# Optimization experiments

Measured on AMD Instinct MI355X. Metric: run time of the kernel, lower is better.

## Reference

```python
import jax, jax.numpy as jnp
import numpy as np

N, E, H, D_IN, D_OUT, DEPTH, G = 100000, 1600000, 128, 128, 10, 3, 256


def setup_inputs() -> dict:
    key = jax.random.key(0)
    ks = jax.random.split(key, 16)
    s = lambda k, shape: jax.random.normal(k, shape, dtype=jnp.float32) * 0.05
    inp = {
        "x": jax.random.normal(ks[0], (N, D_IN), dtype=jnp.float32),
        "edge_index": jax.random.randint(ks[1], (2, E), 0, N, dtype=jnp.int32),
        "control_edge_index": jax.random.randint(ks[2], (2, 1024), 0, N, dtype=jnp.int32),
        "batch": jnp.sort(jax.random.randint(ks[3], (N,), 0, G, dtype=jnp.int32)),
        # encoder MLP: input_dim -> hidden -> hidden
        "enc_w1": s(ks[4], (D_IN, H)), "enc_b1": jnp.zeros((H,), jnp.float32),
        "enc_w2": s(ks[5], (H, H)),    "enc_b2": jnp.zeros((H,), jnp.float32),
        # conv_depth GCN layers, hidden -> hidden
        "conv_w": s(ks[6], (DEPTH, H, H)), "conv_b": jnp.zeros((DEPTH, H), jnp.float32),
        # decoder MLP: hidden -> hidden -> output_dim
        "dec_w1": s(ks[7], (H, H)),     "dec_b1": jnp.zeros((H,), jnp.float32),
        "dec_w2": s(ks[8], (H, D_OUT)), "dec_b2": jnp.zeros((D_OUT,), jnp.float32),
    }
    return inp


def _gcn_forward(x, enc_w1, enc_b1, enc_w2, enc_b2, conv_w, conv_b,
                 dec_w1, dec_b1, dec_w2, dec_b2, edge_index, batch):
    # encoder MLP (Linear-ReLU-Dropout(eval)-Linear)
    h = jax.nn.relu(x @ enc_w1 + enc_b1) @ enc_w2 + enc_b2

    # GCN normalization with self-loops: D^{-1/2} (A + I) D^{-1/2}
    loops = jnp.arange(N, dtype=edge_index.dtype)
    src = jnp.concatenate([edge_index[0], loops])  # [E + N]
    dst = jnp.concatenate([edge_index[1], loops])
    deg = jax.ops.segment_sum(jnp.ones_like(src, dtype=h.dtype), dst, num_segments=N)
    inv_sqrt = jax.lax.rsqrt(deg)  # deg >= 1 thanks to self-loops
    coef = (inv_sqrt[src] * inv_sqrt[dst])[:, None]  # [E+N, 1]

    for l in range(DEPTH):
        hw = h @ conv_w[l] + conv_b[l]                      # [N, H]
        h = jax.ops.segment_sum(hw[src] * coef, dst, num_segments=N)
        if l < DEPTH - 1:  # linear=False -> nonlinearity between convs
            h = jax.nn.relu(h)

    # global_add_pool over graph ids
    pooled = jax.ops.segment_sum(h, batch, num_segments=G)   # [G, H]

    # decoder MLP
    return jax.nn.relu(pooled @ dec_w1 + dec_b1) @ dec_w2 + dec_b2  # [G, D_OUT]


def reference(x, edge_index, control_edge_index, batch, enc_w1, enc_b1, enc_w2,
              enc_b2, conv_w, conv_b, dec_w1, dec_b1, dec_w2, dec_b2):
    # control_edge_index corresponds to the (disabled) control mechanism; unused
    return _gcn_forward(x, enc_w1, enc_b1, enc_w2, enc_b2, conv_w, conv_b,
                        dec_w1, dec_b1, dec_w2, dec_b2, edge_index, batch)
```

## Files before the change

### kernel.cpp

```cpp
#include <hip/hip_runtime.h>
#include <hip/hip_bf16.h>
#include <cstdint>
#include <cstddef>

#define NN 100000
#define NE 1600000
#define HH 128
#define NG 256

#define NB 196
#define BSH 9
#define BMSK 511
#define CHUNK 16384
#define NBLK 98

typedef __bf16 bf16x8 __attribute__((ext_vector_type(8)));
typedef float floatx4 __attribute__((ext_vector_type(4)));

__device__ __forceinline__ uint32_t f2b(float f) {
  union { float f; uint32_t u; } v; v.f = f;
  uint32_t u = v.u;
  return (u + 0x7FFFu + ((u >> 16) & 1u)) >> 16;
}
__device__ __forceinline__ float b2f(uint32_t h) {
  union { uint32_t u; float f; } v; v.u = h << 16;
  return v.f;
}
__device__ __forceinline__ void addrow(float* a, uint4 v) {
  a[0] += b2f(v.x & 0xFFFFu); a[1] += b2f(v.x >> 16);
  a[2] += b2f(v.y & 0xFFFFu); a[3] += b2f(v.y >> 16);
  a[4] += b2f(v.z & 0xFFFFu); a[5] += b2f(v.z >> 16);
  a[6] += b2f(v.w & 0xFFFFu); a[7] += b2f(v.w >> 16);
}

__device__ __forceinline__ void stage_w(uint16_t (*Wt)[136], const float* __restrict__ W,
                                        int tid) {
  for (int it = 0; it < 16; ++it) {
    int idx = tid + it * 256;
    int n = idx & 127;
    int k0 = (idx >> 7) * 4;
    uint2 wv;
    wv.x = f2b(W[(k0 + 0) * 128 + n]) | (f2b(W[(k0 + 1) * 128 + n]) << 16);
    wv.y = f2b(W[(k0 + 2) * 128 + n]) | (f2b(W[(k0 + 3) * 128 + n]) << 16);
    *(uint2*)&Wt[n][k0] = wv;
  }
}


__global__ __launch_bounds__(256) void k_cntA(const int* __restrict__ src,
                                              int* __restrict__ blkcnt) {
  __shared__ int h[NB];
  int t = threadIdx.x;
  if (t < NB) h[t] = 0;
  __syncthreads();
  int base = blockIdx.x * CHUNK, end = min(base + CHUNK, NE);
  for (int i = base + t; i < end; i += 256) atomicAdd(&h[src[i] >> BSH], 1);
  __syncthreads();
  if (t < NB) blkcnt[blockIdx.x * NB + t] = h[t];
}

__global__ __launch_bounds__(256) void k_cntB(const uint2* __restrict__ pairs,
                                              int* __restrict__ blkcnt) {
  __shared__ int h[NB];
  int t = threadIdx.x;
  if (t < NB) h[t] = 0;
  __syncthreads();
  int base = blockIdx.x * CHUNK, end = min(base + CHUNK, NE);
  for (int i = base + t; i < end; i += 256) atomicAdd(&h[pairs[i].y >> BSH], 1);
  __syncthreads();
  if (t < NB) blkcnt[blockIdx.x * NB + t] = h[t];
}

__global__ void k_scan(const int* __restrict__ blkcnt, int* __restrict__ poff,
                       int* __restrict__ gbase, int* __restrict__ off, int set_off) {
  __shared__ int s[256];
  int t = threadIdx.x;
  int tot = 0;
  if (t < NB) {
    for (int r = 0; r < NBLK; ++r) {
      poff[r * NB + t] = tot;
      tot += blkcnt[r * NB + t];
    }
  }
  s[t] = (t < NB) ? tot : 0;
  __syncthreads();
  for (int d = 1; d < 256; d <<= 1) {
    int v = (t >= d) ? s[t - d] : 0;
    __syncthreads();
    s[t] += v;
    __syncthreads();
  }
  if (t < NB) gbase[t] = s[t] - tot;
  if (t == 0) { gbase[NB] = NE; if (set_off) off[NN] = NE; }
}

__global__ __launch_bounds__(256) void k_placeA(const int* __restrict__ src,
                                                const int* __restrict__ dst,
                                                const int* __restrict__ poff,
                                                const int* __restrict__ gbase,
                                                uint2* __restrict__ pairs) {
  __shared__ int cur[NB];
  int t = threadIdx.x;
  if (t < NB) cur[t] = poff[blockIdx.x * NB + t] + gbase[t];
  __syncthreads();
  int base = blockIdx.x * CHUNK, end = min(base + CHUNK, NE);
  for (int i = base + t; i < end; i += 256) {
    int s = src[i], d = dst[i];
    int p = atomicAdd(&cur[s >> BSH], 1);
    pairs[p] = make_uint2((unsigned)s, (unsigned)d);
  }
}

__global__ __launch_bounds__(256) void k_placeB(const uint2* __restrict__ pairs,
                                                const int* __restrict__ poff,
                                                const int* __restrict__ gbase,
                                                uint32_t* __restrict__ outb) {
  __shared__ int cur[NB];
  int t = threadIdx.x;
  if (t < NB) cur[t] = poff[blockIdx.x * NB + t] + gbase[t];
  __syncthreads();
  int base = blockIdx.x * CHUNK, end = min(base + CHUNK, NE);
  for (int i = base + t; i < end; i += 256) {
    uint2 v = pairs[i];
    int p = atomicAdd(&cur[v.y >> BSH], 1);
    outb[p] = v.x | ((v.y & (unsigned)BMSK) << 17);
  }
}

__global__ __launch_bounds__(256) void k_bucket_sort(
    const uint32_t* __restrict__ pairbuf, const int* __restrict__ gbase,
    const int* __restrict__ batch,
    int* __restrict__ off, float* __restrict__ inv, int* __restrict__ csrs,
    int* __restrict__ dhist2, int* __restrict__ gstart)
{
  __shared__ int cnt[512];
  __shared__ int loff[512];
  __shared__ int psum[256];
  int b = blockIdx.x;
  int tid = threadIdx.x;
  cnt[tid] = 0; cnt[tid + 256] = 0;
  __syncthreads();
  int s0 = gbase[b], s1 = gbase[b + 1];
  for (int i = s0 + tid; i < s1; i += 256)
    atomicAdd(&cnt[pairbuf[i] >> 17], 1);
  __syncthreads();
  int a0 = cnt[2 * tid], a1 = cnt[2 * tid + 1];
  int s = a0 + a1;
  psum[tid] = s;
  __syncthreads();
  for (int d = 1; d < 256; d <<= 1) {
    int v = (tid >= d) ? psum[tid - d] : 0;
    __syncthreads();
    psum[tid] += v;
    __syncthreads();
  }
  int excl = psum[tid] - s;
  loff[2 * tid] = excl;
  loff[2 * tid + 1] = excl + a0;
  __syncthreads();
  int* h64 = psum;
  if (tid < 64) h64[tid] = 0;
  __syncthreads();
#pragma unroll
  for (int k = 0; k < 2; ++k) {
    int i = tid + k * 256;
    int node = b * 512 + i;
    if (node < NN) {
      off[node] = s0 + loff[i];
      inv[node] = rsqrtf((float)cnt[i] + 1.0f);
      int d = cnt[i]; if (d > 63) d = 63;
      atomicAdd(&h64[d], 1);
    }
  }
  {
    int n0 = b * 512, n1 = min(n0 + 512, NN);
    for (int i = n0 + tid; i < n1; i += 256) {
      int bb = batch[i];
      if (i == 0) { for (int g = 0; g <= bb; ++g) gstart[g] = 0; }
      else { int aa = batch[i - 1]; for (int g = aa + 1; g <= bb; ++g) gstart[g] = i; }
      if (i == NN - 1) { for (int g = bb + 1; g <= NG; ++g) gstart[g] = NN; }
    }
  }
  __syncthreads();
  if (tid < 64) dhist2[b * 64 + tid] = h64[tid];
  cnt[tid] = loff[tid]; cnt[tid + 256] = loff[tid + 256];
  __syncthreads();
  for (int i = s0 + tid; i < s1; i += 256) {
    uint32_t v = pairbuf[i];
    int p = atomicAdd(&cnt[v >> 17], 1);
    csrs[s0 + p] = (int)(v & 0x1FFFFu);
  }
}

__global__ void k_dscan(const int* __restrict__ dhist2, int* __restrict__ dcur) {
  int t = threadIdx.x;
  int sum = 0;
  for (int r = 0; r < NB; ++r) sum += dhist2[r * 64 + (63 - t)];
  int v = sum;
  for (int d = 1; d < 64; d <<= 1) { int u = __shfl_up(v, d); if (t >= d) v += u; }
  dcur[63 - t] = v - sum;
}

__global__ __launch_bounds__(256) void k_dplace(const int* __restrict__ off,
                                                int* __restrict__ dcur,
                                                int* __restrict__ order) {
  __shared__ int h[64], base[64];
  int t = threadIdx.x;
  if (t < 64) h[t] = 0;
  __syncthreads();
  int i = blockIdx.x * 256 + t;
  int d = 0, ld = 0;
  if (i < NN) { d = off[i + 1] - off[i]; if (d > 63) d = 63; ld = atomicAdd(&h[d], 1); }
  __syncthreads();
  if (t < 64) base[t] = h[t] ? atomicAdd(&dcur[t], h[t]) : 0;
  __syncthreads();
  if (i < NN) order[base[d] + ld] = i;
}

__global__ __launch_bounds__(256) void k_gemm(
    const uint16_t* __restrict__ A16, const float* __restrict__ A32,
    const float* __restrict__ W, const float* __restrict__ bias,
    const float* __restrict__ scale,
    uint16_t* __restrict__ Out, int M, int do_relu)
{
  __shared__ uint16_t Wt[128][136];
  const int tid = threadIdx.x;
  stage_w(Wt, W, tid);
  __syncthreads();

  const int lane = tid & 63;
  const int wave = tid >> 6;
  const int lrow = lane & 15;
  const int quad = lane >> 4;
  const int lk = quad * 8;
  const int row0 = blockIdx.x * 128 + wave * 32;

  floatx4 acc[2][8];
#pragma unroll
  for (int t = 0; t < 2; ++t)
#pragma unroll
    for (int n = 0; n < 8; ++n)
      acc[t][n] = (floatx4){0.f, 0.f, 0.f, 0.f};

#pragma unroll
  for (int ks = 0; ks < 4; ++ks) {
    bf16x8 a[2];
#pragma unroll
    for (int t = 0; t < 2; ++t) {
      int r = row0 + t * 16 + lrow;
      uint4 tmp = {0u, 0u, 0u, 0u};
      if (r < M) {
        if (A32) {
          float4 f0 = *(const float4*)(A32 + (size_t)r * HH + ks * 32 + lk);
          float4 f1 = *(const float4*)(A32 + (size_t)r * HH + ks * 32 + lk + 4);
          tmp.x = f2b(f0.x) | (f2b(f0.y) << 16);
          tmp.y = f2b(f0.z) | (f2b(f0.w) << 16);
          tmp.z = f2b(f1.x) | (f2b(f1.y) << 16);
          tmp.w = f2b(f1.z) | (f2b(f1.w) << 16);
        } else {
          tmp = *(const uint4*)(A16 + (size_t)r * HH + ks * 32 + lk);
        }
      }
      a[t] = __builtin_bit_cast(bf16x8, tmp);
    }
#pragma unroll
    for (int n = 0; n < 8; ++n) {
      bf16x8 b = __builtin_bit_cast(bf16x8, *(const uint4*)&Wt[n * 16 + lrow][ks * 32 + lk]);
      acc[0][n] = __builtin_amdgcn_mfma_f32_16x16x32_bf16(b, a[0], acc[0][n], 0, 0, 0);
      acc[1][n] = __builtin_amdgcn_mfma_f32_16x16x32_bf16(b, a[1], acc[1][n], 0, 0, 0);
    }
  }

  float4 b4[8];
#pragma unroll
  for (int n = 0; n < 8; ++n) b4[n] = *(const float4*)(bias + n * 16 + quad * 4);

#pragma unroll
  for (int t = 0; t < 2; ++t) {
    int row = row0 + t * 16 + lrow;
    if (row < M) {
      float sc = scale ? scale[row] : 1.0f;
      uint16_t* orow = Out + (size_t)row * HH;
#pragma unroll
      for (int n = 0; n < 8; ++n) {
        float v0 = acc[t][n][0] + b4[n].x;
        float v1 = acc[t][n][1] + b4[n].y;
        float v2 = acc[t][n][2] + b4[n].z;
        float v3 = acc[t][n][3] + b4[n].w;
        if (do_relu) {
          v0 = fmaxf(v0, 0.f); v1 = fmaxf(v1, 0.f);
          v2 = fmaxf(v2, 0.f); v3 = fmaxf(v3, 0.f);
        }
        v0 *= sc; v1 *= sc; v2 *= sc; v3 *= sc;
        uint2 o;
        o.x = f2b(v0) | (f2b(v1) << 16);
        o.y = f2b(v2) | (f2b(v3) << 16);
        *(uint2*)(orow + n * 16 + quad * 4) = o;
      }
    }
  }
}

__global__ __launch_bounds__(256) void k_gemm_dual(
    const uint16_t* __restrict__ A16,
    const float* __restrict__ Wa, const float* __restrict__ ba,
    const float* __restrict__ Wb, const float* __restrict__ bb,
    const float* __restrict__ scale,
    uint16_t* __restrict__ Out, int M)
{
  __shared__ uint16_t Wt[128][136];
  __shared__ uint16_t tile[128][136];
  const int tid = threadIdx.x;
  stage_w(Wt, Wa, tid);
  __syncthreads();

  const int lane = tid & 63;
  const int wave = tid >> 6;
  const int lrow = lane & 15;
  const int quad = lane >> 4;
  const int lk = quad * 8;
  const int row0 = blockIdx.x * 128 + wave * 32;
  const int trow0 = wave * 32;

  floatx4 acc[2][8];
#pragma unroll
  for (int t = 0; t < 2; ++t)
#pragma unroll
    for (int n = 0; n < 8; ++n)
      acc[t][n] = (floatx4){0.f, 0.f, 0.f, 0.f};

#pragma unroll
  for (int ks = 0; ks < 4; ++ks) {
    bf16x8 a[2];
#pragma unroll
    for (int t = 0; t < 2; ++t) {
      int r = row0 + t * 16 + lrow;
      uint4 tmp = {0u, 0u, 0u, 0u};
      if (r < M) tmp = *(const uint4*)(A16 + (size_t)r * HH + ks * 32 + lk);
      a[t] = __builtin_bit_cast(bf16x8, tmp);
    }
#pragma unroll
    for (int n = 0; n < 8; ++n) {
      bf16x8 b = __builtin_bit_cast(bf16x8, *(const uint4*)&Wt[n * 16 + lrow][ks * 32 + lk]);
      acc[0][n] = __builtin_amdgcn_mfma_f32_16x16x32_bf16(b, a[0], acc[0][n], 0, 0, 0);
      acc[1][n] = __builtin_amdgcn_mfma_f32_16x16x32_bf16(b, a[1], acc[1][n], 0, 0, 0);
    }
  }

  {
    float4 b4[8];
#pragma unroll
    for (int n = 0; n < 8; ++n) b4[n] = *(const float4*)(ba + n * 16 + quad * 4);
#pragma unroll
    for (int t = 0; t < 2; ++t) {
      int trow = trow0 + t * 16 + lrow;
#pragma unroll
      for (int n = 0; n < 8; ++n) {
        uint2 o;
        o.x = f2b(acc[t][n][0] + b4[n].x) | (f2b(acc[t][n][1] + b4[n].y) << 16);
        o.y = f2b(acc[t][n][2] + b4[n].z) | (f2b(acc[t][n][3] + b4[n].w) << 16);
        *(uint2*)&tile[trow][n * 16 + quad * 4] = o;
      }
    }
  }
  __syncthreads();
  stage_w(Wt, Wb, tid);
#pragma unroll
  for (int t = 0; t < 2; ++t)
#pragma unroll
    for (int n = 0; n < 8; ++n)
      acc[t][n] = (floatx4){0.f, 0.f, 0.f, 0.f};
  __syncthreads();

#pragma unroll
  for (int ks = 0; ks < 4; ++ks) {
    bf16x8 a[2];
#pragma unroll
    for (int t = 0; t < 2; ++t)
      a[t] = __builtin_bit_cast(bf16x8,
               *(const uint4*)&tile[trow0 + t * 16 + lrow][ks * 32 + lk]);
#pragma unroll
    for (int n = 0; n < 8; ++n) {
      bf16x8 b = __builtin_bit_cast(bf16x8, *(const uint4*)&Wt[n * 16 + lrow][ks * 32 + lk]);
      acc[0][n] = __builtin_amdgcn_mfma_f32_16x16x32_bf16(b, a[0], acc[0][n], 0, 0, 0);
      acc[1][n] = __builtin_amdgcn_mfma_f32_16x16x32_bf16(b, a[1], acc[1][n], 0, 0, 0);
    }
  }

  {
    float4 b4[8];
#pragma unroll
    for (int n = 0; n < 8; ++n) b4[n] = *(const float4*)(bb + n * 16 + quad * 4);
#pragma unroll
    for (int t = 0; t < 2; ++t) {
      int row = row0 + t * 16 + lrow;
      if (row < M) {
        float sc = scale ? scale[row] : 1.0f;
        uint16_t* orow = Out + (size_t)row * HH;
#pragma unroll
        for (int n = 0; n < 8; ++n) {
          float v0 = (acc[t][n][0] + b4[n].x) * sc;
          float v1 = (acc[t][n][1] + b4[n].y) * sc;
          float v2 = (acc[t][n][2] + b4[n].z) * sc;
          float v3 = (acc[t][n][3] + b4[n].w) * sc;
          uint2 o;
          o.x = f2b(v0) | (f2b(v1) << 16);
          o.y = f2b(v2) | (f2b(v3) << 16);
          *(uint2*)(orow + n * 16 + quad * 4) = o;
        }
      }
    }
  }
}

__global__ __launch_bounds__(256) void k_agg(
    const uint16_t* __restrict__ hw2, const int* __restrict__ off,
    const int* __restrict__ csrs, const float* __restrict__ inv,
    const int* __restrict__ order,
    uint16_t* __restrict__ hout, int do_relu)
{
  int slot = blockIdx.x * 16 + (threadIdx.x >> 4);
  if (slot >= NN) return;
  int node = order[slot];
  int c = (threadIdx.x & 15) * 8;

  uint4 sv = *(const uint4*)(hw2 + (size_t)node * HH + c);
  float a[8] = {0.f, 0.f, 0.f, 0.f, 0.f, 0.f, 0.f, 0.f};
  addrow(a, sv);

  int e0 = off[node], e1 = off[node + 1];
  int e = e0;
  for (; e + 4 <= e1; e += 4) {
    int s0 = csrs[e + 0], s1 = csrs[e + 1], s2 = csrs[e + 2], s3 = csrs[e + 3];
    uint4 v0 = *(const uint4*)(hw2 + (size_t)s0 * HH + c);
    uint4 v1 = *(const uint4*)(hw2 + (size_t)s1 * HH + c);
    uint4 v2 = *(const uint4*)(hw2 + (size_t)s2 * HH + c);
    uint4 v3 = *(const uint4*)(hw2 + (size_t)s3 * HH + c);
    addrow(a, v0); addrow(a, v1); addrow(a, v2); addrow(a, v3);
  }
  for (; e < e1; ++e) {
    int s = csrs[e];
    uint4 v = *(const uint4*)(hw2 + (size_t)s * HH + c);
    addrow(a, v);
  }
  float invd = inv[node];
#pragma unroll
  for (int j = 0; j < 8; ++j) {
    a[j] *= invd;
    if (do_relu) a[j] = fmaxf(a[j], 0.f);
  }
  uint4 o;
  o.x = f2b(a[0]) | (f2b(a[1]) << 16);
  o.y = f2b(a[2]) | (f2b(a[3]) << 16);
  o.z = f2b(a[4]) | (f2b(a[5]) << 16);
  o.w = f2b(a[6]) | (f2b(a[7]) << 16);
  *(uint4*)(hout + (size_t)node * HH + c) = o;
}

__global__ __launch_bounds__(256) void k_pooldec(
    const uint16_t* __restrict__ h, const int* __restrict__ gstart,
    const float* __restrict__ w1, const float* __restrict__ b1,
    const float* __restrict__ w2, const float* __restrict__ b2,
    float* __restrict__ out)
{
  __shared__ float red[16][132];
  __shared__ float p[128], tmpv[128];
  int g = blockIdx.x;
  int tid = threadIdx.x;
  int slot = tid >> 4;
  int c = (tid & 15) * 8;

  int r0 = gstart[g], r1 = gstart[g + 1];
  float a[8] = {0.f, 0.f, 0.f, 0.f, 0.f, 0.f, 0.f, 0.f};
  for (int r = r0 + slot; r < r1; r += 16) {
    uint4 v = *(const uint4*)(h + (size_t)r * HH + c);
    a[0] += b2f(v.x & 0xFFFFu); a[1] += b2f(v.x >> 16);
    a[2] += b2f(v.y & 0xFFFFu); a[3] += b2f(v.y >> 16);
    a[4] += b2f(v.z & 0xFFFFu); a[5] += b2f(v.z >> 16);
    a[6] += b2f(v.w & 0xFFFFu); a[7] += b2f(v.w >> 16);
  }
  *(float4*)&red[slot][c]     = make_float4(a[0], a[1], a[2], a[3]);
  *(float4*)&red[slot][c + 4] = make_float4(a[4], a[5], a[6], a[7]);
  __syncthreads();
  if (tid < 128) {
    float s = 0.f;
#pragma unroll
    for (int k = 0; k < 16; ++k) s += red[k][tid];
    p[tid] = s;
  }
  __syncthreads();
  if (tid < 128) {
    float acc1 = b1[tid];
    for (int k = 0; k < 128; ++k) acc1 += p[k] * w1[k * 128 + tid];
    tmpv[tid] = fmaxf(acc1, 0.f);
  }
  __syncthreads();
  if (tid < 10) {
    float o = b2[tid];
    for (int k = 0; k < 128; ++k) o += tmpv[k] * w2[k * 10 + tid];
    out[g * 10 + tid] = o;
  }
}

extern "C" void kernel_launch(void* const* d_in, const int* in_sizes, int n_in,
                              void* d_out, int out_size, void* d_ws, size_t ws_size,
                              hipStream_t stream) {
  const float* x       = (const float*)d_in[0];
  const int*   eidx    = (const int*)d_in[1];
  const int*   src     = eidx;
  const int*   dst     = eidx + NE;
  const int*   batch   = (const int*)d_in[3];
  const float* enc_w1  = (const float*)d_in[4];
  const float* enc_b1  = (const float*)d_in[5];
  const float* enc_w2  = (const float*)d_in[6];
  const float* enc_b2  = (const float*)d_in[7];
  const float* conv_w  = (const float*)d_in[8];
  const float* conv_b  = (const float*)d_in[9];
  const float* dec_w1  = (const float*)d_in[10];
  const float* dec_b1  = (const float*)d_in[11];
  const float* dec_w2  = (const float*)d_in[12];
  const float* dec_b2  = (const float*)d_in[13];
  float* out = (float*)d_out;

  char* ws = (char*)d_ws;
  size_t o = 0;
  auto alloc = [&](size_t bytes) -> char* {
    char* p = ws + o;
    o += (bytes + 255) & ~(size_t)255;
    return p;
  };
  int*      off     = (int*)alloc((size_t)(NN + 1) * 4);
  int*      csrs    = (int*)alloc((size_t)NE * 4);
  float*    inv     = (float*)alloc((size_t)NN * 4);
  int*      blkcntA = (int*)alloc((size_t)NBLK * NB * 4);
  int*      poffA   = (int*)alloc((size_t)NBLK * NB * 4);
  int*      blkcntB = (int*)alloc((size_t)NBLK * NB * 4);
  int*      poffB   = (int*)alloc((size_t)NBLK * NB * 4);
  int*      gbaseA  = (int*)alloc((size_t)(NB + 1) * 4);
  int*      gbaseB  = (int*)alloc((size_t)(NB + 1) * 4);
  int*      dhist2  = (int*)alloc((size_t)NB * 64 * 4);
  int*      dcur    = (int*)alloc(64 * 4);
  int*      order   = (int*)alloc((size_t)NN * 4);
  int*      gstart  = (int*)alloc((size_t)(NG + 1) * 4);
  uint16_t* buf0    = (uint16_t*)alloc((size_t)NN * HH * 2);
  uint16_t* buf1    = (uint16_t*)alloc((size_t)NN * HH * 2);
  uint2*    pairsA  = (uint2*)buf1;
  uint32_t* pairB   = (uint32_t*)((char*)buf1 + (size_t)NE * 8);

  k_cntA<<<dim3(NBLK), dim3(256), 0, stream>>>(src, blkcntA);
  k_scan<<<dim3(1), dim3(256), 0, stream>>>(blkcntA, poffA, gbaseA, off, 0);
  k_placeA<<<dim3(NBLK), dim3(256), 0, stream>>>(src, dst, poffA, gbaseA, pairsA);
  k_cntB<<<dim3(NBLK), dim3(256), 0, stream>>>(pairsA, blkcntB);
  k_scan<<<dim3(1), dim3(256), 0, stream>>>(blkcntB, poffB, gbaseB, off, 1);
  k_placeB<<<dim3(NBLK), dim3(256), 0, stream>>>(pairsA, poffB, gbaseB, pairB);
  k_bucket_sort<<<dim3(NB), dim3(256), 0, stream>>>(pairB, gbaseB, batch, off, inv, csrs,
                                                    dhist2, gstart);

  const int NBK = (NN + 255) / 256;
  k_dscan<<<dim3(1), dim3(64), 0, stream>>>(dhist2, dcur);
  k_dplace<<<dim3(NBK), dim3(256), 0, stream>>>(off, dcur, order);

  const int GB = (NN + 127) / 128;
  k_gemm<<<dim3(GB), dim3(256), 0, stream>>>(nullptr, x, enc_w1, enc_b1, nullptr, buf1, NN, 1);
  k_gemm_dual<<<dim3(GB), dim3(256), 0, stream>>>(buf1, enc_w2, enc_b2,
                                                  conv_w + 0 * 16384, conv_b + 0,
                                                  inv, buf0, NN);

  const int AB = (NN + 15) / 16;
  k_agg <<<dim3(AB), dim3(256), 0, stream>>>(buf0, off, csrs, inv, order, buf1, 1);
  k_gemm<<<dim3(GB), dim3(256), 0, stream>>>(buf1, nullptr, conv_w + 1 * 16384, conv_b + 128, inv, buf0, NN, 0);
  k_agg <<<dim3(AB), dim3(256), 0, stream>>>(buf0, off, csrs, inv, order, buf1, 1);
  k_gemm<<<dim3(GB), dim3(256), 0, stream>>>(buf1, nullptr, conv_w + 2 * 16384, conv_b + 256, inv, buf0, NN, 0);
  k_agg <<<dim3(AB), dim3(256), 0, stream>>>(buf0, off, csrs, inv, order, buf1, 0);

  k_pooldec<<<dim3(NG), dim3(256), 0, stream>>>(buf1, gstart, dec_w1, dec_b1, dec_w2, dec_b2, out);
}
```

Baseline: 517.8 us.

## Store node features in 16-column slabs so aggregation gathers stay cache-local

Node feature buffers move from row-major [N,128] to eight column slabs of [N,16] bf16. The GEMM loads, GEMM stores and pooling reads are remapped to match. The aggregation kernel now runs eight block groups, one per slab, with two lanes per node, so each pass's random gather touches only a 3.2MB slab that can stay in cache. It also uses inline-asm sc0 loads, nontemporal index loads and stores, and index sharing through shuffles. The cost is re-reading the CSR eight times, and the inline asm waits on every group of four loads, which limits memory-level parallelism.

```diff
diff --git a/kernel.cpp b/kernel.cpp
--- a/kernel.cpp
+++ b/kernel.cpp
@@ -14,8 +14,11 @@
 #define CHUNK 16384
 #define NBLK 98
 
+#define SLAB16 ((size_t)NN * 16)
+
 typedef __bf16 bf16x8 __attribute__((ext_vector_type(8)));
 typedef float floatx4 __attribute__((ext_vector_type(4)));
+typedef uint32_t u32x4 __attribute__((ext_vector_type(4)));
 
 __device__ __forceinline__ uint32_t f2b(float f) {
   union { float f; uint32_t u; } v; v.f = f;
@@ -26,11 +29,32 @@
   union { uint32_t u; float f; } v; v.u = h << 16;
   return v.f;
 }
-__device__ __forceinline__ void addrow(float* a, uint4 v) {
-  a[0] += b2f(v.x & 0xFFFFu); a[1] += b2f(v.x >> 16);
-  a[2] += b2f(v.y & 0xFFFFu); a[3] += b2f(v.y >> 16);
-  a[4] += b2f(v.z & 0xFFFFu); a[5] += b2f(v.z >> 16);
-  a[6] += b2f(v.w & 0xFFFFu); a[7] += b2f(v.w >> 16);
+__device__ __forceinline__ void addrow(float* a, u32x4 v) {
+  a[0] += b2f(v[0] & 0xFFFFu); a[1] += b2f(v[0] >> 16);
+  a[2] += b2f(v[1] & 0xFFFFu); a[3] += b2f(v[1] >> 16);
+  a[4] += b2f(v[2] & 0xFFFFu); a[5] += b2f(v[2] >> 16);
+  a[6] += b2f(v[3] & 0xFFFFu); a[7] += b2f(v[3] >> 16);
+}
+
+__device__ __forceinline__ u32x4 ld16_sc0(const uint16_t* p) {
+  u32x4 v;
+  asm volatile("global_load_dwordx4 %0, %1, off sc0\n\t"
+               "s_waitcnt vmcnt(0)"
+               : "=v"(v) : "v"(p) : "memory");
+  return v;
+}
+__device__ __forceinline__ void ld16x4_sc0(const uint16_t* p0, const uint16_t* p1,
+                                           const uint16_t* p2, const uint16_t* p3,
+                                           u32x4& v0, u32x4& v1, u32x4& v2, u32x4& v3) {
+  asm volatile(
+      "global_load_dwordx4 %0, %4, off sc0\n\t"
+      "global_load_dwordx4 %1, %5, off sc0\n\t"
+      "global_load_dwordx4 %2, %6, off sc0\n\t"
+      "global_load_dwordx4 %3, %7, off sc0\n\t"
+      "s_waitcnt vmcnt(0)"
+      : "=&v"(v0), "=&v"(v1), "=&v"(v2), "=&v"(v3)
+      : "v"(p0), "v"(p1), "v"(p2), "v"(p3)
+      : "memory");
 }
 
 __device__ __forceinline__ void stage_w(uint16_t (*Wt)[136], const float* __restrict__ W,
@@ -258,7 +282,8 @@
           tmp.z = f2b(f1.x) | (f2b(f1.y) << 16);
           tmp.w = f2b(f1.z) | (f2b(f1.w) << 16);
         } else {
-          tmp = *(const uint4*)(A16 + (size_t)r * HH + ks * 32 + lk);
+          tmp = *(const uint4*)(A16 + ((size_t)(ks * 2 + (quad >> 1)) * NN + r) * 16
+                                + (quad & 1) * 8);
         }
       }
       a[t] = __builtin_bit_cast(bf16x8, tmp);
@@ -280,7 +305,6 @@
     int row = row0 + t * 16 + lrow;
     if (row < M) {
       float sc = scale ? scale[row] : 1.0f;
-      uint16_t* orow = Out + (size_t)row * HH;
 #pragma unroll
       for (int n = 0; n < 8; ++n) {
         float v0 = acc[t][n][0] + b4[n].x;
@@ -295,7 +319,7 @@
         uint2 o;
         o.x = f2b(v0) | (f2b(v1) << 16);
         o.y = f2b(v2) | (f2b(v3) << 16);
-        *(uint2*)(orow + n * 16 + quad * 4) = o;
+        *(uint2*)(Out + ((size_t)n * NN + row) * 16 + quad * 4) = o;
       }
     }
   }
@@ -336,7 +360,9 @@
     for (int t = 0; t < 2; ++t) {
       int r = row0 + t * 16 + lrow;
       uint4 tmp = {0u, 0u, 0u, 0u};
-      if (r < M) tmp = *(const uint4*)(A16 + (size_t)r * HH + ks * 32 + lk);
+      if (r < M)
+        tmp = *(const uint4*)(A16 + ((size_t)(ks * 2 + (quad >> 1)) * NN + r) * 16
+                              + (quad & 1) * 8);
       a[t] = __builtin_bit_cast(bf16x8, tmp);
     }
 #pragma unroll
@@ -396,7 +422,6 @@
       int row = row0 + t * 16 + lrow;
       if (row < M) {
         float sc = scale ? scale[row] : 1.0f;
-        uint16_t* orow = Out + (size_t)row * HH;
 #pragma unroll
         for (int n = 0; n < 8; ++n) {
           float v0 = (acc[t][n][0] + b4[n].x) * sc;
@@ -406,7 +431,7 @@
           uint2 o;
           o.x = f2b(v0) | (f2b(v1) << 16);
           o.y = f2b(v2) | (f2b(v3) << 16);
-          *(uint2*)(orow + n * 16 + quad * 4) = o;
+          *(uint2*)(Out + ((size_t)n * NN + row) * 16 + quad * 4) = o;
         }
       }
     }
@@ -419,42 +444,47 @@
     const int* __restrict__ order,
     uint16_t* __restrict__ hout, int do_relu)
 {
-  int slot = blockIdx.x * 16 + (threadIdx.x >> 4);
+  const int g = blockIdx.x & 7;
+  const int slot = (blockIdx.x >> 3) * 128 + (threadIdx.x >> 1);
   if (slot >= NN) return;
-  int node = order[slot];
-  int c = (threadIdx.x & 15) * 8;
-
-  uint4 sv = *(const uint4*)(hw2 + (size_t)node * HH + c);
+  const int p = threadIdx.x & 1;
+  const int node = order[slot];
+
+  const uint16_t* base = hw2 + (size_t)g * SLAB16;
   float a[8] = {0.f, 0.f, 0.f, 0.f, 0.f, 0.f, 0.f, 0.f};
-  addrow(a, sv);
-
-  int e0 = off[node], e1 = off[node + 1];
+
+  addrow(a, ld16_sc0(base + (size_t)node * 16 + p * 8));
+
+  const int e0 = off[node], e1 = off[node + 1];
   int e = e0;
   for (; e + 4 <= e1; e += 4) {
-    int s0 = csrs[e + 0], s1 = csrs[e + 1], s2 = csrs[e + 2], s3 = csrs[e + 3];
-    uint4 v0 = *(const uint4*)(hw2 + (size_t)s0 * HH + c);
-    uint4 v1 = *(const uint4*)(hw2 + (size_t)s1 * HH + c);
-    uint4 v2 = *(const uint4*)(hw2 + (size_t)s2 * HH + c);
-    uint4 v3 = *(const uint4*)(hw2 + (size_t)s3 * HH + c);
+    int i0 = __builtin_nontemporal_load(csrs + e + 2 * p);
+    int i1 = __builtin_nontemporal_load(csrs + e + 2 * p + 1);
+    int j0 = __shfl_xor(i0, 1);
+    int j1 = __shfl_xor(i1, 1);
+    u32x4 v0, v1, v2, v3;
+    ld16x4_sc0(base + (size_t)i0 * 16 + p * 8, base + (size_t)i1 * 16 + p * 8,
+               base + (size_t)j0 * 16 + p * 8, base + (size_t)j1 * 16 + p * 8,
+               v0, v1, v2, v3);
     addrow(a, v0); addrow(a, v1); addrow(a, v2); addrow(a, v3);
   }
   for (; e < e1; ++e) {
-    int s = csrs[e];
-    uint4 v = *(const uint4*)(hw2 + (size_t)s * HH + c);
-    addrow(a, v);
-  }
+    int s = __builtin_nontemporal_load(csrs + e);
+    addrow(a, ld16_sc0(base + (size_t)s * 16 + p * 8));
+  }
+
   float invd = inv[node];
 #pragma unroll
   for (int j = 0; j < 8; ++j) {
     a[j] *= invd;
     if (do_relu) a[j] = fmaxf(a[j], 0.f);
   }
-  uint4 o;
-  o.x = f2b(a[0]) | (f2b(a[1]) << 16);
-  o.y = f2b(a[2]) | (f2b(a[3]) << 16);
-  o.z = f2b(a[4]) | (f2b(a[5]) << 16);
-  o.w = f2b(a[6]) | (f2b(a[7]) << 16);
-  *(uint4*)(hout + (size_t)node * HH + c) = o;
+  u32x4 o;
+  o[0] = f2b(a[0]) | (f2b(a[1]) << 16);
+  o[1] = f2b(a[2]) | (f2b(a[3]) << 16);
+  o[2] = f2b(a[4]) | (f2b(a[5]) << 16);
+  o[3] = f2b(a[6]) | (f2b(a[7]) << 16);
+  __builtin_nontemporal_store(o, (u32x4*)(hout + (size_t)g * SLAB16 + (size_t)node * 16 + p * 8));
 }
 
 __global__ __launch_bounds__(256) void k_pooldec(
@@ -469,11 +499,12 @@
   int tid = threadIdx.x;
   int slot = tid >> 4;
   int c = (tid & 15) * 8;
+  const uint16_t* hp = h + (size_t)(c >> 4) * SLAB16 + (c & 15);
 
   int r0 = gstart[g], r1 = gstart[g + 1];
   float a[8] = {0.f, 0.f, 0.f, 0.f, 0.f, 0.f, 0.f, 0.f};
   for (int r = r0 + slot; r < r1; r += 16) {
-    uint4 v = *(const uint4*)(h + (size_t)r * HH + c);
+    uint4 v = *(const uint4*)(hp + (size_t)r * 16);
     a[0] += b2f(v.x & 0xFFFFu); a[1] += b2f(v.x >> 16);
     a[2] += b2f(v.y & 0xFFFFu); a[3] += b2f(v.y >> 16);
     a[4] += b2f(v.z & 0xFFFFu); a[5] += b2f(v.z >> 16);
@@ -566,12 +597,12 @@
                                                   conv_w + 0 * 16384, conv_b + 0,
                                                   inv, buf0, NN);
 
-  const int AB = (NN + 15) / 16;
-  k_agg <<<dim3(AB), dim3(256), 0, stream>>>(buf0, off, csrs, inv, order, buf1, 1);
+  const int AGB = 8 * ((NN + 127) / 128);
+  k_agg <<<dim3(AGB), dim3(256), 0, stream>>>(buf0, off, csrs, inv, order, buf1, 1);
   k_gemm<<<dim3(GB), dim3(256), 0, stream>>>(buf1, nullptr, conv_w + 1 * 16384, conv_b + 128, inv, buf0, NN, 0);
-  k_agg <<<dim3(AB), dim3(256), 0, stream>>>(buf0, off, csrs, inv, order, buf1, 1);
+  k_agg <<<dim3(AGB), dim3(256), 0, stream>>>(buf0, off, csrs, inv, order, buf1, 1);
   k_gemm<<<dim3(GB), dim3(256), 0, stream>>>(buf1, nullptr, conv_w + 2 * 16384, conv_b + 256, inv, buf0, NN, 0);
-  k_agg <<<dim3(AB), dim3(256), 0, stream>>>(buf0, off, csrs, inv, order, buf1, 0);
+  k_agg <<<dim3(AGB), dim3(256), 0, stream>>>(buf0, off, csrs, inv, order, buf1, 0);
 
   k_pooldec<<<dim3(NG), dim3(256), 0, stream>>>(buf1, gstart, dec_w1, dec_b1, dec_w2, dec_b2, out);
 }
```

Measured after the change: 880.1 us. +70.0%, slower.
